# Performance work log

Hardware: AMD Instinct MI355X
Metric: run time of the kernel (lower is better)

## Reference

```python
import jax, jax.numpy as jnp
import numpy as np

N = 2048
IN_FEAT = 256
OUT_FEAT = 64
E_FEAT = 32
NHID = 64
ALPHA = 0.2
NHEADS = 4
NLAYERS = 3
NEG_INF = -9e15


def setup_inputs() -> dict:
    key = jax.random.key(0)
    ks = jax.random.split(key, 6)
    x = jax.random.normal(ks[0], (N, IN_FEAT), dtype=jnp.float32)
    adj = jax.random.randint(ks[1], (N, N), 0, 2, dtype=jnp.int32)
    e = jax.random.normal(ks[2], (N, N, E_FEAT), dtype=jnp.float32)
    # All layers share shapes because in_feat == nhid*nheads and out_feat == nhid.
    # xavier-ish scale
    W_e = jax.random.normal(ks[3], (NLAYERS, NHEADS, E_FEAT, IN_FEAT), dtype=jnp.float32) * (1.414 * (2.0 / (E_FEAT + IN_FEAT)) ** 0.5)
    W = jax.random.normal(ks[4], (NLAYERS, NHEADS, IN_FEAT, NHID), dtype=jnp.float32) * (1.414 * (2.0 / (IN_FEAT + NHID)) ** 0.5)
    a = jax.random.normal(ks[5], (NLAYERS, NHEADS, 3 * NHID), dtype=jnp.float32) * (1.414 * (2.0 / (3 * NHID + 1)) ** 0.5)
    return {"x": x, "adj": adj, "e": e, "W_e": W_e, "W": W, "a": a}


def reference(x, adj, e, W_e, W, a):
    # dropout = 0.0 / eval mode -> identity
    out = W.shape[-1]
    nlayers = W.shape[0]
    mask = (adj > 0)[None]  # [1, N, N], broadcast over heads
    for l in range(nlayers):
        islast = (l == nlayers - 1)
        h = jnp.einsum('ni,hio->hno', x, W[l])  # [H, N, out]
        a1 = a[l, :, :out]            # [H, out]
        a2 = a[l, :, out:2 * out]     # [H, out]
        a3 = a[l, :, 2 * out:]        # [H, out]
        # score_ij = leakyrelu(a1.h_i + a2.h_j + a3.(e_ij @ W_e @ W))
        coef = jnp.einsum('heo,ho->he', jnp.einsum('hei,hio->heo', W_e[l], W[l]), a3)  # [H, E_FEAT]
        e_score = jnp.einsum('nmf,hf->hnm', e, coef)  # [H, N, N]
        s1 = jnp.einsum('hno,ho->hn', h, a1)[:, :, None]
        s2 = jnp.einsum('hno,ho->hn', h, a2)[:, None, :]
        score = jax.nn.leaky_relu(s1 + s2 + e_score, ALPHA)
        att = jax.nn.softmax(jnp.where(mask, score, NEG_INF), axis=-1)
        h_prime = jnp.einsum('hnm,hmo->hno', att, h)  # [H, N, out]
        if islast:
            x = jax.nn.elu(h_prime.mean(axis=0))  # [N, out]
        else:
            # concat heads along feature dim (head-major), with per-head elu
            x = jnp.transpose(jax.nn.elu(h_prime), (1, 0, 2)).reshape(h_prime.shape[1], -1)
    return x
```

## Files before the change

kernel.cpp:

```cpp
#include <hip/hip_runtime.h>
#include <cstdint>
#include <cstddef>

#define Nn 2048
#define FIN 256
#define EFEAT 32
#define HID 64
#define NH 4
#define NL 3
#define LRELU_A 0.2f

typedef _Float16 h4 __attribute__((ext_vector_type(4)));
typedef _Float16 h8 __attribute__((ext_vector_type(8)));
typedef float f4 __attribute__((ext_vector_type(4)));

#define NEGH ((_Float16)(-60000.0f))

__global__ void k_coef(const float* __restrict__ W, const float* __restrict__ We,
                       const float* __restrict__ a, float* __restrict__ coef) {
  int lh = blockIdx.x;
  int t = threadIdx.x;
  __shared__ float tl[FIN];
  const float* Wb = W + (size_t)lh * FIN * HID;
  const float* ab = a + (size_t)lh * (3 * HID) + 2 * HID;
  float acc = 0.f;
#pragma unroll 8
  for (int o = 0; o < HID; ++o) acc = fmaf(Wb[(size_t)t * HID + o], ab[o], acc);
  tl[t] = acc;
  __syncthreads();
  if (t < EFEAT) {
    const float* Web = We + ((size_t)lh * EFEAT + t) * FIN;
    float c = 0.f;
    for (int i = 0; i < FIN; ++i) c = fmaf(Web[i], tl[i], c);
    coef[lh * EFEAT + t] = c;
  }
}

template <int C>
__global__ __launch_bounds__(256) void k_escore(
    const float* __restrict__ e, const int* __restrict__ adj,
    const float* __restrict__ coef, _Float16* __restrict__ es) {
  size_t idx = (size_t)blockIdx.x * 256 + threadIdx.x;
  int m = (int)(idx & (Nn - 1));
  int n = (int)(idx >> 11);
  int mt = m >> 5, ml = m & 31;
  const size_t cstride = (size_t)64 * Nn * 32;
  size_t sbase = ((size_t)mt * Nn + n) * 32 + (size_t)ml;
  int aj = adj[idx];
  if (aj == 0) {
#pragma unroll
    for (int c = 0; c < C; ++c) es[(size_t)c * cstride + sbase] = NEGH;
    return;
  }
  const float4* ep = (const float4*)(e + idx * EFEAT);
  float evv[EFEAT];
#pragma unroll
  for (int g = 0; g < 8; ++g) {
    float4 v = ep[g];
    evv[g * 4 + 0] = v.x; evv[g * 4 + 1] = v.y; evv[g * 4 + 2] = v.z; evv[g * 4 + 3] = v.w;
  }
#pragma clang loop unroll(disable)
  for (int c = 0; c < C; ++c) {
    const float* cf = coef + c * EFEAT;
    float acc = 0.f;
#pragma unroll
    for (int f = 0; f < EFEAT; ++f) acc = fmaf(evv[f], cf[f], acc);
    es[(size_t)c * cstride + sbase] = (_Float16)acc;
  }
}

__global__ __launch_bounds__(256) void k_h(
    const float* __restrict__ x, const float* __restrict__ W,
    const float* __restrict__ a, int layer,
    _Float16* __restrict__ hT, float* __restrict__ s1, float* __restrict__ s2) {
  int t = threadIdx.x;
  int n0 = blockIdx.x * 8;
  int h = t >> 6, o = t & 63;
  const float* Wb = W + ((size_t)(layer * NH + h) * FIN) * HID + o;
  const float* xb = x + (size_t)n0 * FIN;
  float acc[8] = {};
  for (int i0 = 0; i0 < FIN; i0 += 4) {
    float w0 = Wb[(size_t)(i0 + 0) * HID];
    float w1 = Wb[(size_t)(i0 + 1) * HID];
    float w2 = Wb[(size_t)(i0 + 2) * HID];
    float w3 = Wb[(size_t)(i0 + 3) * HID];
#pragma unroll
    for (int j = 0; j < 8; ++j) {
      float4 xv = *(const float4*)(xb + (size_t)j * FIN + i0);
      acc[j] = fmaf(xv.x, w0, acc[j]);
      acc[j] = fmaf(xv.y, w1, acc[j]);
      acc[j] = fmaf(xv.z, w2, acc[j]);
      acc[j] = fmaf(xv.w, w3, acc[j]);
    }
  }
  const float* ab = a + (size_t)(layer * NH + h) * (3 * HID);
  float a1v = ab[o], a2v = ab[HID + o];
#pragma unroll
  for (int j = 0; j < 8; ++j) {
    float r1 = acc[j] * a1v, r2 = acc[j] * a2v;
#pragma unroll
    for (int d = 1; d < 64; d <<= 1) {
      r1 += __shfl_xor(r1, d, 64);
      r2 += __shfl_xor(r2, d, 64);
    }
    if (o == 0) { s1[h * Nn + n0 + j] = r1; s2[h * Nn + n0 + j] = r2; }
  }
  int mt = n0 >> 5, ml = n0 & 31;
  h8 hv;
#pragma unroll
  for (int j = 0; j < 8; ++j) hv[j] = (_Float16)acc[j];
  *(h8*)(hT + (((size_t)h * 64 + mt) * 64 + o) * 32 + ml) = hv;
}

__global__ __launch_bounds__(256) void k_attn(
    const _Float16* __restrict__ es, const _Float16* __restrict__ hT,
    const float* __restrict__ s1, const float* __restrict__ s2,
    float* __restrict__ hp, int layer) {
  int h = blockIdx.x;
  int n0 = blockIdx.y * 16;
  int t = threadIdx.x;
  int w = t >> 6;
  int l = t & 63;
  int col = l & 15, grp = l >> 4;
  int n = n0 + col;
  float s1v = s1[h * Nn + n];
  const _Float16* esb = es + (size_t)(layer * NH + h) * ((size_t)64 * Nn * 32);
  const _Float16* hTb = hT + (size_t)h * ((size_t)64 * 64 * 32);
  const float* s2b = s2 + h * Nn;

  float M = -3.0e38f, S = 0.f;
  f4 acc[4] = {};

  for (int c16 = 0; c16 < 32; ++c16) {
    int m0 = w * 512 + c16 * 16;
    int mt = m0 >> 5;
    int ml0 = (m0 & 31) + grp * 4;
    h4 ev = *(const h4*)(esb + ((size_t)mt * Nn + n) * 32 + ml0);
    float4 sv = *(const float4*)(s2b + m0 + grp * 4);
    float sc0 = s1v + sv.x + (float)ev[0]; sc0 = fmaxf(sc0, LRELU_A * sc0);
    float sc1 = s1v + sv.y + (float)ev[1]; sc1 = fmaxf(sc1, LRELU_A * sc1);
    float sc2 = s1v + sv.z + (float)ev[2]; sc2 = fmaxf(sc2, LRELU_A * sc2);
    float sc3 = s1v + sv.w + (float)ev[3]; sc3 = fmaxf(sc3, LRELU_A * sc3);
    float cm = fmaxf(fmaxf(sc0, sc1), fmaxf(sc2, sc3));
    cm = fmaxf(cm, __shfl_xor(cm, 16, 64));
    cm = fmaxf(cm, __shfl_xor(cm, 32, 64));
    float Mn = fmaxf(M, cm);
    float fac = __expf(M - Mn);
    M = Mn;
    S *= fac;
#pragma unroll
    for (int ot = 0; ot < 4; ++ot) acc[ot] *= fac;
    h4 pb;
    pb[0] = (_Float16)__expf(sc0 - Mn);
    pb[1] = (_Float16)__expf(sc1 - Mn);
    pb[2] = (_Float16)__expf(sc2 - Mn);
    pb[3] = (_Float16)__expf(sc3 - Mn);
    S += (float)pb[0] + (float)pb[1] + (float)pb[2] + (float)pb[3];
    const _Float16* hp0 = hTb + ((size_t)mt * 64 + col) * 32 + ml0;
#pragma unroll
    for (int ot = 0; ot < 4; ++ot) {
      h4 af = *(const h4*)(hp0 + (size_t)ot * 16 * 32);
      acc[ot] = __builtin_amdgcn_mfma_f32_16x16x16f16(af, pb, acc[ot], 0, 0, 0);
    }
  }

  S += __shfl_xor(S, 16, 64);
  S += __shfl_xor(S, 32, 64);

  __shared__ float red[4][16][64];
  __shared__ float Mw[4][16];
  __shared__ float Sw[4][16];
  if (l < 16) { Mw[w][l] = M; Sw[w][l] = S; }
#pragma unroll
  for (int ot = 0; ot < 4; ++ot)
    *(f4*)&red[w][col][ot * 16 + grp * 4] = acc[ot];
  __syncthreads();

  int nl = t >> 4, o0 = (t & 15) * 4;
  float Ms = fmaxf(fmaxf(Mw[0][nl], Mw[1][nl]), fmaxf(Mw[2][nl], Mw[3][nl]));
  float Ssum = 0.f;
  f4 v = {};
#pragma unroll
  for (int ww = 0; ww < 4; ++ww) {
    float f = __expf(Mw[ww][nl] - Ms);
    Ssum = fmaf(Sw[ww][nl], f, Ssum);
    f4 r = *(const f4*)&red[ww][nl][o0];
    v += r * f;
  }
  float is = 1.0f / Ssum;
  *(f4*)(hp + ((size_t)h * Nn + n0 + nl) * HID + o0) = v * is;
}

__global__ void k_xnext(const float* __restrict__ hp, float* __restrict__ xn) {
  int idx = blockIdx.x * 256 + threadIdx.x;
  int n = idx >> 8, rem = idx & 255;
  int h = rem >> 6, o = rem & 63;
  float v = hp[((size_t)h * Nn + n) * HID + o];
  xn[idx] = v > 0.f ? v : expm1f(v);
}

__global__ void k_out(const float* __restrict__ hp, float* __restrict__ out) {
  int idx = blockIdx.x * 256 + threadIdx.x;
  int n = idx >> 6, o = idx & 63;
  size_t b = (size_t)n * HID + o;
  float v = 0.25f * (hp[b] + hp[(size_t)Nn * HID + b] +
                     hp[2 * (size_t)Nn * HID + b] + hp[3 * (size_t)Nn * HID + b]);
  out[idx] = v > 0.f ? v : expm1f(v);
}

extern "C" void kernel_launch(void* const* d_in, const int* in_sizes, int n_in,
                              void* d_out, int out_size, void* d_ws, size_t ws_size,
                              hipStream_t stream) {
  const float* x_in = (const float*)d_in[0];
  const int* adj = (const int*)d_in[1];
  const float* e = (const float*)d_in[2];
  const float* We = (const float*)d_in[3];
  const float* W = (const float*)d_in[4];
  const float* a = (const float*)d_in[5];
  float* out = (float*)d_out;

  char* ws = (char*)d_ws;
  size_t off = 0;
  auto alloc = [&](size_t bytes) -> void* {
    off = (off + 255) & ~(size_t)255;
    void* p = ws + off;
    off += bytes;
    return p;
  };
  float* coef = (float*)alloc((size_t)NL * NH * EFEAT * sizeof(float));
  float* s1 = (float*)alloc((size_t)NH * Nn * sizeof(float));
  float* s2 = (float*)alloc((size_t)NH * Nn * sizeof(float));
  float* hp = (float*)alloc((size_t)NH * Nn * HID * sizeof(float));
  float* xA = (float*)alloc((size_t)Nn * FIN * sizeof(float));
  float* xB = (float*)alloc((size_t)Nn * FIN * sizeof(float));
  _Float16* hT = (_Float16*)alloc((size_t)NH * 64 * 64 * 32 * sizeof(_Float16));
  _Float16* es = (_Float16*)alloc((size_t)NL * NH * 64 * Nn * 32 * sizeof(_Float16));

  hipLaunchKernelGGL(k_coef, dim3(NL * NH), dim3(256), 0, stream, W, We, a, coef);

  size_t total = (size_t)Nn * Nn;
  hipLaunchKernelGGL((k_escore<NL * NH>), dim3((unsigned)(total / 256)), dim3(256), 0, stream,
                     e, adj, coef, es);

  for (int l = 0; l < NL; ++l) {
    const float* xcur = (l == 0) ? x_in : ((l == 1) ? xA : xB);
    hipLaunchKernelGGL(k_h, dim3(Nn / 8), dim3(256), 0, stream, xcur, W, a, l, hT, s1, s2);
    hipLaunchKernelGGL(k_attn, dim3(NH, Nn / 16), dim3(256), 0, stream,
                       es, hT, s1, s2, hp, l);
    if (l == NL - 1) {
      hipLaunchKernelGGL(k_out, dim3(Nn * HID / 256), dim3(256), 0, stream, hp, out);
    } else {
      float* xn = (l == 0) ? xA : xB;
      hipLaunchKernelGGL(k_xnext, dim3(Nn * FIN / 256), dim3(256), 0, stream, hp, xn);
    }
  }
}
```

Baseline: 279.2 us.

## Widen attention to 8 waves, fuse ELU into attention, lazily rescale softmax

The attention kernel now runs 512 threads (8 waves), each wave covering 256 key columns. The edge-score and hT tile layout changes from 32-wide to 64-wide tiles to match. The per-layer ELU/transpose kernel is folded into the attention epilogue, and the online-softmax rescale runs only when some lane's max increases. The edge-score kernel drops its early-return branch so every thread follows the same store path. The cost is more shared memory per block, more divergence in the reduction epilogue, and extra e-score arithmetic for masked entries.

```diff
diff --git a/kernel.cpp b/kernel.cpp
--- a/kernel.cpp
+++ b/kernel.cpp
@@ -43,21 +43,18 @@
   size_t idx = (size_t)blockIdx.x * 256 + threadIdx.x;
   int m = (int)(idx & (Nn - 1));
   int n = (int)(idx >> 11);
-  int mt = m >> 5, ml = m & 31;
-  const size_t cstride = (size_t)64 * Nn * 32;
-  size_t sbase = ((size_t)mt * Nn + n) * 32 + (size_t)ml;
+  int mt = m >> 6, ml = m & 63;
+  const size_t cstride = (size_t)32 * Nn * 64;
+  size_t sbase = ((size_t)mt * Nn + n) * 64 + (size_t)ml;
   int aj = adj[idx];
-  if (aj == 0) {
-#pragma unroll
-    for (int c = 0; c < C; ++c) es[(size_t)c * cstride + sbase] = NEGH;
-    return;
-  }
-  const float4* ep = (const float4*)(e + idx * EFEAT);
-  float evv[EFEAT];
-#pragma unroll
-  for (int g = 0; g < 8; ++g) {
-    float4 v = ep[g];
-    evv[g * 4 + 0] = v.x; evv[g * 4 + 1] = v.y; evv[g * 4 + 2] = v.z; evv[g * 4 + 3] = v.w;
+  float evv[EFEAT] = {};
+  if (aj != 0) {
+    const float4* ep = (const float4*)(e + idx * EFEAT);
+#pragma unroll
+    for (int g = 0; g < 8; ++g) {
+      float4 v = ep[g];
+      evv[g * 4 + 0] = v.x; evv[g * 4 + 1] = v.y; evv[g * 4 + 2] = v.z; evv[g * 4 + 3] = v.w;
+    }
   }
 #pragma clang loop unroll(disable)
   for (int c = 0; c < C; ++c) {
@@ -65,7 +62,7 @@
     float acc = 0.f;
 #pragma unroll
     for (int f = 0; f < EFEAT; ++f) acc = fmaf(evv[f], cf[f], acc);
-    es[(size_t)c * cstride + sbase] = (_Float16)acc;
+    es[(size_t)c * cstride + sbase] = aj ? (_Float16)acc : NEGH;
   }
 }
 
@@ -105,17 +102,17 @@
     }
     if (o == 0) { s1[h * Nn + n0 + j] = r1; s2[h * Nn + n0 + j] = r2; }
   }
-  int mt = n0 >> 5, ml = n0 & 31;
+  int mt = n0 >> 6, ml = n0 & 63;
   h8 hv;
 #pragma unroll
   for (int j = 0; j < 8; ++j) hv[j] = (_Float16)acc[j];
-  *(h8*)(hT + (((size_t)h * 64 + mt) * 64 + o) * 32 + ml) = hv;
-}
-
-__global__ __launch_bounds__(256) void k_attn(
+  *(h8*)(hT + (((size_t)h * 32 + mt) * 64 + o) * 64 + ml) = hv;
+}
+
+__global__ __launch_bounds__(512) void k_attn(
     const _Float16* __restrict__ es, const _Float16* __restrict__ hT,
     const float* __restrict__ s1, const float* __restrict__ s2,
-    float* __restrict__ hp, int layer) {
+    float* __restrict__ hp, float* __restrict__ xn, int layer, int last) {
   int h = blockIdx.x;
   int n0 = blockIdx.y * 16;
   int t = threadIdx.x;
@@ -124,18 +121,18 @@
   int col = l & 15, grp = l >> 4;
   int n = n0 + col;
   float s1v = s1[h * Nn + n];
-  const _Float16* esb = es + (size_t)(layer * NH + h) * ((size_t)64 * Nn * 32);
-  const _Float16* hTb = hT + (size_t)h * ((size_t)64 * 64 * 32);
+  const _Float16* esb = es + (size_t)(layer * NH + h) * ((size_t)32 * Nn * 64);
+  const _Float16* hTb = hT + (size_t)h * ((size_t)32 * 64 * 64);
   const float* s2b = s2 + h * Nn;
 
   float M = -3.0e38f, S = 0.f;
   f4 acc[4] = {};
 
-  for (int c16 = 0; c16 < 32; ++c16) {
-    int m0 = w * 512 + c16 * 16;
-    int mt = m0 >> 5;
-    int ml0 = (m0 & 31) + grp * 4;
-    h4 ev = *(const h4*)(esb + ((size_t)mt * Nn + n) * 32 + ml0);
+  for (int c16 = 0; c16 < 16; ++c16) {
+    int m0 = w * 256 + c16 * 16;
+    int mt = m0 >> 6;
+    int ml0 = (m0 & 63) + grp * 4;
+    h4 ev = *(const h4*)(esb + ((size_t)mt * Nn + n) * 64 + ml0);
     float4 sv = *(const float4*)(s2b + m0 + grp * 4);
     float sc0 = s1v + sv.x + (float)ev[0]; sc0 = fmaxf(sc0, LRELU_A * sc0);
     float sc1 = s1v + sv.y + (float)ev[1]; sc1 = fmaxf(sc1, LRELU_A * sc1);
@@ -144,22 +141,24 @@
     float cm = fmaxf(fmaxf(sc0, sc1), fmaxf(sc2, sc3));
     cm = fmaxf(cm, __shfl_xor(cm, 16, 64));
     cm = fmaxf(cm, __shfl_xor(cm, 32, 64));
-    float Mn = fmaxf(M, cm);
-    float fac = __expf(M - Mn);
-    M = Mn;
-    S *= fac;
-#pragma unroll
-    for (int ot = 0; ot < 4; ++ot) acc[ot] *= fac;
+    if (__any(cm > M)) {
+      float Mn = fmaxf(M, cm);
+      float fac = __expf(M - Mn);
+      M = Mn;
+      S *= fac;
+#pragma unroll
+      for (int ot = 0; ot < 4; ++ot) acc[ot] *= fac;
+    }
     h4 pb;
-    pb[0] = (_Float16)__expf(sc0 - Mn);
-    pb[1] = (_Float16)__expf(sc1 - Mn);
-    pb[2] = (_Float16)__expf(sc2 - Mn);
-    pb[3] = (_Float16)__expf(sc3 - Mn);
+    pb[0] = (_Float16)__expf(sc0 - M);
+    pb[1] = (_Float16)__expf(sc1 - M);
+    pb[2] = (_Float16)__expf(sc2 - M);
+    pb[3] = (_Float16)__expf(sc3 - M);
     S += (float)pb[0] + (float)pb[1] + (float)pb[2] + (float)pb[3];
-    const _Float16* hp0 = hTb + ((size_t)mt * 64 + col) * 32 + ml0;
+    const _Float16* hp0 = hTb + ((size_t)mt * 64 + col) * 64 + ml0;
 #pragma unroll
     for (int ot = 0; ot < 4; ++ot) {
-      h4 af = *(const h4*)(hp0 + (size_t)ot * 16 * 32);
+      h4 af = *(const h4*)(hp0 + (size_t)ot * 16 * 64);
       acc[ot] = __builtin_amdgcn_mfma_f32_16x16x16f16(af, pb, acc[ot], 0, 0, 0);
     }
   }
@@ -167,36 +166,40 @@
   S += __shfl_xor(S, 16, 64);
   S += __shfl_xor(S, 32, 64);
 
-  __shared__ float red[4][16][64];
-  __shared__ float Mw[4][16];
-  __shared__ float Sw[4][16];
+  __shared__ float red[8][16][64];
+  __shared__ float Mw[8][16];
+  __shared__ float Sw[8][16];
   if (l < 16) { Mw[w][l] = M; Sw[w][l] = S; }
 #pragma unroll
   for (int ot = 0; ot < 4; ++ot)
     *(f4*)&red[w][col][ot * 16 + grp * 4] = acc[ot];
   __syncthreads();
 
-  int nl = t >> 4, o0 = (t & 15) * 4;
-  float Ms = fmaxf(fmaxf(Mw[0][nl], Mw[1][nl]), fmaxf(Mw[2][nl], Mw[3][nl]));
-  float Ssum = 0.f;
-  f4 v = {};
-#pragma unroll
-  for (int ww = 0; ww < 4; ++ww) {
-    float f = __expf(Mw[ww][nl] - Ms);
-    Ssum = fmaf(Sw[ww][nl], f, Ssum);
-    f4 r = *(const f4*)&red[ww][nl][o0];
-    v += r * f;
-  }
-  float is = 1.0f / Ssum;
-  *(f4*)(hp + ((size_t)h * Nn + n0 + nl) * HID + o0) = v * is;
-}
-
-__global__ void k_xnext(const float* __restrict__ hp, float* __restrict__ xn) {
-  int idx = blockIdx.x * 256 + threadIdx.x;
-  int n = idx >> 8, rem = idx & 255;
-  int h = rem >> 6, o = rem & 63;
-  float v = hp[((size_t)h * Nn + n) * HID + o];
-  xn[idx] = v > 0.f ? v : expm1f(v);
+  if (t < 256) {
+    int nl = t >> 4, o0 = (t & 15) * 4;
+    float Ms = Mw[0][nl];
+#pragma unroll
+    for (int ww = 1; ww < 8; ++ww) Ms = fmaxf(Ms, Mw[ww][nl]);
+    float Ssum = 0.f;
+    f4 v = {};
+#pragma unroll
+    for (int ww = 0; ww < 8; ++ww) {
+      float f = __expf(Mw[ww][nl] - Ms);
+      Ssum = fmaf(Sw[ww][nl], f, Ssum);
+      f4 r = *(const f4*)&red[ww][nl][o0];
+      v += r * f;
+    }
+    float is = 1.0f / Ssum;
+    v *= is;
+    if (last) {
+      *(f4*)(hp + ((size_t)h * Nn + n0 + nl) * HID + o0) = v;
+    } else {
+      f4 xo;
+#pragma unroll
+      for (int k = 0; k < 4; ++k) xo[k] = v[k] > 0.f ? v[k] : expm1f(v[k]);
+      *(f4*)(xn + (size_t)(n0 + nl) * FIN + h * HID + o0) = xo;
+    }
+  }
 }
 
 __global__ void k_out(const float* __restrict__ hp, float* __restrict__ out) {
@@ -233,8 +236,8 @@
   float* hp = (float*)alloc((size_t)NH * Nn * HID * sizeof(float));
   float* xA = (float*)alloc((size_t)Nn * FIN * sizeof(float));
   float* xB = (float*)alloc((size_t)Nn * FIN * sizeof(float));
-  _Float16* hT = (_Float16*)alloc((size_t)NH * 64 * 64 * 32 * sizeof(_Float16));
-  _Float16* es = (_Float16*)alloc((size_t)NL * NH * 64 * Nn * 32 * sizeof(_Float16));
+  _Float16* hT = (_Float16*)alloc((size_t)NH * 32 * 64 * 64 * sizeof(_Float16));
+  _Float16* es = (_Float16*)alloc((size_t)NL * NH * 32 * Nn * 64 * sizeof(_Float16));
 
   hipLaunchKernelGGL(k_coef, dim3(NL * NH), dim3(256), 0, stream, W, We, a, coef);
 
@@ -244,14 +247,10 @@
 
   for (int l = 0; l < NL; ++l) {
     const float* xcur = (l == 0) ? x_in : ((l == 1) ? xA : xB);
+    float* xn = (l == 0) ? xA : xB;
     hipLaunchKernelGGL(k_h, dim3(Nn / 8), dim3(256), 0, stream, xcur, W, a, l, hT, s1, s2);
-    hipLaunchKernelGGL(k_attn, dim3(NH, Nn / 16), dim3(256), 0, stream,
-                       es, hT, s1, s2, hp, l);
-    if (l == NL - 1) {
-      hipLaunchKernelGGL(k_out, dim3(Nn * HID / 256), dim3(256), 0, stream, hp, out);
-    } else {
-      float* xn = (l == 0) ? xA : xB;
-      hipLaunchKernelGGL(k_xnext, dim3(Nn * FIN / 256), dim3(256), 0, stream, hp, xn);
-    }
-  }
-}
+    hipLaunchKernelGGL(k_attn, dim3(NH, Nn / 16), dim3(512), 0, stream,
+                       es, hT, s1, s2, hp, xn, l, l == NL - 1 ? 1 : 0);
+  }
+  hipLaunchKernelGGL(k_out, dim3(Nn * HID / 256), dim3(256), 0, stream, hp, out);
+}
```

Result: slower. 311.3 us (+11.5%).
